# Kernel tuning notes

Measured on AMD Instinct MI355X. Metric: run time of the kernel, lower is better.

Reference implementation:

```python
import jax, jax.numpy as jnp
import numpy as np

D_MODEL = 1024
N_HEADS = 16
HEAD_DIM = D_MODEL // N_HEADS  # 64; used only as softmax scale in windowed path
WINDOW = 128


def _window_starts(seq_len, window):
    # Faithful to the torch loop: stride = window//2, last window right-aligned.
    starts = []
    for i in range(0, seq_len, window // 2):
        end = min(i + window, seq_len)
        starts.append(max(0, end - window))
        if end == seq_len:
            break
    return np.asarray(starts, dtype=np.int32)


def setup_inputs() -> dict:
    key = jax.random.key(0)
    ks = jax.random.split(key, 9)
    B, S = 4, 4096
    sc = 1.0 / np.sqrt(D_MODEL)
    return {
        "x": jax.random.normal(ks[0], (B, S, D_MODEL), jnp.float32),
        "Wq": jax.random.normal(ks[1], (D_MODEL, D_MODEL), jnp.float32) * sc,
        "bq": jax.random.normal(ks[2], (D_MODEL,), jnp.float32) * 0.02,
        "Wk": jax.random.normal(ks[3], (D_MODEL, D_MODEL), jnp.float32) * sc,
        "bk": jax.random.normal(ks[4], (D_MODEL,), jnp.float32) * 0.02,
        "Wv": jax.random.normal(ks[5], (D_MODEL, D_MODEL), jnp.float32) * sc,
        "bv": jax.random.normal(ks[6], (D_MODEL,), jnp.float32) * 0.02,
        "Wo": jax.random.normal(ks[7], (D_MODEL, D_MODEL), jnp.float32) * sc,
        "bo": jax.random.normal(ks[8], (D_MODEL,), jnp.float32) * 0.02,
    }


def reference(x, Wq, bq, Wk, bk, Wv, bv, Wo, bo):
    B, S, D = x.shape
    q = x @ Wq + bq  # [B,S,D]
    k = x @ Wk + bk
    v = x @ Wv + bv

    # Overlapping sliding windows (heads merged, as in the original windowed path).
    starts = _window_starts(S, WINDOW)                      # [W]
    idx = starts[:, None] + np.arange(WINDOW)[None, :]      # [W, w] static
    idx_j = jnp.asarray(idx)
    qw = q[:, idx_j]  # [B, W, w, D]
    kw = k[:, idx_j]
    vw = v[:, idx_j]
    scores = jnp.einsum('bwqd,bwkd->bwqk', qw, kw) / np.sqrt(HEAD_DIM)
    attn = jax.nn.softmax(scores, axis=-1)
    out_w = jnp.einsum('bwqk,bwkd->bwqd', attn, vw)         # [B, W, w, D]

    # Overlap-add then average by coverage counts.
    flat_idx = idx.reshape(-1)
    out = jnp.zeros((B, S, D), x.dtype).at[:, flat_idx].add(
        out_w.reshape(B, -1, D))
    counts = jnp.zeros((S,), x.dtype).at[flat_idx].add(1.0)
    out = out / counts[None, :, None]

    return out @ Wo + bo
```

## Files before the change

kernel.cpp:

```cpp
#include <hip/hip_runtime.h>
#include <stdint.h>
#include <stddef.h>

#define D_MODEL 1024
#define SEQ     4096
#define BATCH   4
#define MTOT    (BATCH*SEQ)
#define NWIN    63

typedef __bf16 bf16;
typedef __bf16 bf16x8 __attribute__((ext_vector_type(8)));
typedef __bf16 bf16x4 __attribute__((ext_vector_type(4)));
typedef float  floatx4 __attribute__((ext_vector_type(4)));

__device__ __forceinline__ void async_ld16(const void* g, void* l) {
  __builtin_amdgcn_global_load_lds(
      (const __attribute__((address_space(1))) unsigned int*)g,
      (__attribute__((address_space(3))) unsigned int*)l,
      16, 0, 0);
}


__global__ __launch_bounds__(256)
void cvt_x_kernel(const float* __restrict__ x, bf16* __restrict__ xb)
{
  const int i = blockIdx.x * 256 + threadIdx.x;
  const float4 v = ((const float4*)x)[i];
  bf16x4 o = { (bf16)v.x, (bf16)v.y, (bf16)v.z, (bf16)v.w };
  ((bf16x4*)xb)[i] = o;
}

__global__ __launch_bounds__(256)
void cvt_wt_kernel(const float* __restrict__ W0, const float* __restrict__ W1,
                   const float* __restrict__ W2, const float* __restrict__ W3,
                   bf16* __restrict__ wt)
{
  __shared__ float tile[32][33];
  const float* Wsel = (blockIdx.z == 0) ? W0 : (blockIdx.z == 1) ? W1
                    : (blockIdx.z == 2) ? W2 : W3;
  bf16* Wt = wt + (size_t)blockIdx.z * D_MODEL * D_MODEL;
  const int tx = threadIdx.x & 31, ty = threadIdx.x >> 5;
  const int tn = blockIdx.x * 32, tk = blockIdx.y * 32;
#pragma unroll
  for (int j = 0; j < 32; j += 8)
    tile[ty + j][tx] = Wsel[(size_t)(tk + ty + j) * D_MODEL + (tn + tx)];
  __syncthreads();
#pragma unroll
  for (int j = 0; j < 32; j += 8)
    Wt[(size_t)(tn + ty + j) * D_MODEL + (tk + tx)] = (bf16)tile[tx][ty + j];
}

__device__ __forceinline__ void gemm_core_lds(const bf16* __restrict__ A,
                                              const bf16* __restrict__ Bt,
                                              int m0, int n0,
                                              bf16* As, bf16* Bs,
                                              floatx4 (&acc)[4][4],
                                              int w, int l)
{
  const int ll = l & 15, lh = l >> 4;
  const int wm = w >> 1, wn = w & 1;

  const bf16* Abase = A  + (size_t)(m0 + ll) * D_MODEL + lh * 8;
  const bf16* Bbase = Bt + (size_t)(n0 + ll) * D_MODEL + lh * 8;

  for (int t = 0; t < 16; ++t) {
    const int k0 = t << 6;
#pragma unroll
    for (int i = 0; i < 4; ++i) {
      const int f = w * 4 + i;
      const int mt = f & 7, kk = f >> 3;
      async_ld16(Abase + (size_t)(mt * 16) * D_MODEL + (k0 + kk * 32),
                 &As[f * 512 + l * 8]);
      async_ld16(Bbase + (size_t)(mt * 16) * D_MODEL + (k0 + kk * 32),
                 &Bs[f * 512 + l * 8]);
    }
    __syncthreads();
#pragma unroll
    for (int kk = 0; kk < 2; ++kk) {
      bf16x8 af[4], bfr[4];
#pragma unroll
      for (int tt = 0; tt < 4; ++tt) {
        af[tt]  = *(const bf16x8*)&As[(kk * 8 + wm * 4 + tt) * 512 + l * 8];
        bfr[tt] = *(const bf16x8*)&Bs[(kk * 8 + wn * 4 + tt) * 512 + l * 8];
      }
#pragma unroll
      for (int mt = 0; mt < 4; ++mt)
#pragma unroll
        for (int nt = 0; nt < 4; ++nt)
          acc[mt][nt] = __builtin_amdgcn_mfma_f32_16x16x32_bf16(af[mt], bfr[nt], acc[mt][nt], 0, 0, 0);
    }
    __syncthreads();
  }
}

__global__ __launch_bounds__(256)
void gemm_qkv(const bf16* __restrict__ A, const bf16* __restrict__ Bt,
              const float* __restrict__ bq, const float* __restrict__ bk,
              const float* __restrict__ bv,
              bf16* __restrict__ qo, bf16* __restrict__ ko, bf16* __restrict__ vto)
{
  __shared__ __attribute__((aligned(16))) bf16 As[8192];
  __shared__ __attribute__((aligned(16))) bf16 Bs[8192];
  const int tid = threadIdx.x;
  const int w = tid >> 6, l = tid & 63;
  const int ll = l & 15, lh = l >> 4;
  const int wm = w >> 1, wn = w & 1;

  const int idx = blockIdx.x;
  const int xcd = idx & 7;
  const int local = idx >> 3;
  const int msub = local & 3;
  const int nblk = (local >> 2) % 24;
  const int sub  = local / 96;
  const int mblk = xcd * 16 + sub * 4 + msub;
  const int m0 = mblk * 128, n0 = nblk * 128;

  floatx4 acc[4][4];
#pragma unroll
  for (int i = 0; i < 4; ++i)
#pragma unroll
    for (int j = 0; j < 4; ++j) acc[i][j] = (floatx4)0.f;

  gemm_core_lds(A, Bt, m0, n0, As, Bs, acc, w, l);

  const int sel = n0 >> 10;
  const int ncl = n0 & 1023;
  const float* bias = (sel == 0) ? bq : (sel == 1) ? bk : bv;

#pragma unroll
  for (int mt = 0; mt < 4; ++mt) {
#pragma unroll
    for (int nt = 0; nt < 4; ++nt) {
      const int colL = ncl + wn * 64 + nt * 16 + ll;
      const float bvv = bias[colL];
#pragma unroll
      for (int r = 0; r < 4; ++r) {
        const int row = m0 + wm * 64 + mt * 16 + lh * 4 + r;
        const float v = acc[mt][nt][r] + bvv;
        if (sel == 0) {
          qo[(size_t)row * D_MODEL + colL] = (bf16)v;
        } else if (sel == 1) {
          ko[(size_t)row * D_MODEL + colL] = (bf16)v;
        } else {
          const int bb = row >> 12, s = row & 4095;
          vto[((size_t)bb * D_MODEL + colL) * SEQ + s] = (bf16)v;
        }
      }
    }
  }
}

__global__ __launch_bounds__(256)
void gemm_out(const bf16* __restrict__ A, const bf16* __restrict__ Bt,
              const float* __restrict__ bias, float* __restrict__ C)
{
  __shared__ __attribute__((aligned(16))) bf16 As[8192];
  __shared__ __attribute__((aligned(16))) bf16 Bs[8192];
  const int tid = threadIdx.x;
  const int w = tid >> 6, l = tid & 63;
  const int ll = l & 15, lh = l >> 4;
  const int wm = w >> 1, wn = w & 1;

  const int idx = blockIdx.x;
  const int xcd = idx & 7;
  const int local = idx >> 3;
  const int msub = local & 3;
  const int nblk = (local >> 2) & 7;
  const int sub  = local >> 5;
  const int mblk = xcd * 16 + sub * 4 + msub;
  const int m0 = mblk * 128, n0 = nblk * 128;

  floatx4 acc[4][4];
#pragma unroll
  for (int i = 0; i < 4; ++i)
#pragma unroll
    for (int j = 0; j < 4; ++j) acc[i][j] = (floatx4)0.f;

  gemm_core_lds(A, Bt, m0, n0, As, Bs, acc, w, l);

#pragma unroll
  for (int mt = 0; mt < 4; ++mt) {
#pragma unroll
    for (int nt = 0; nt < 4; ++nt) {
      const int col = n0 + wn * 64 + nt * 16 + ll;
      const float bvv = bias[col];
#pragma unroll
      for (int r = 0; r < 4; ++r) {
        const int row = m0 + wm * 64 + mt * 16 + lh * 4 + r;
        C[(size_t)row * D_MODEL + col] = acc[mt][nt][r] + bvv;
      }
    }
  }
}

__global__ __launch_bounds__(256)
void qk_softmax(const bf16* __restrict__ qb, const bf16* __restrict__ kb,
                bf16* __restrict__ Pg)
{
  __shared__ __attribute__((aligned(16))) bf16 As[4096];
  __shared__ __attribute__((aligned(16))) bf16 Bs[8192];
  __shared__ float redM[4][64];
  __shared__ float redS[4][64];

  const int tid = threadIdx.x;
  const int w = tid >> 6, l = tid & 63, ll = l & 15, lh = l >> 4;
  const int wh = blockIdx.x;
  const int win = wh >> 1, half = wh & 1;
  const int b = blockIdx.y;

  const bf16* Aq = qb + ((size_t)b * SEQ + win * 64 + half * 64) * D_MODEL
                 + (size_t)ll * D_MODEL + lh * 8;
  const bf16* Ak = kb + ((size_t)b * SEQ + win * 64) * D_MODEL
                 + (size_t)ll * D_MODEL + lh * 8;

  floatx4 acc[4][2];
#pragma unroll
  for (int i = 0; i < 4; ++i)
#pragma unroll
    for (int j = 0; j < 2; ++j) acc[i][j] = (floatx4)0.f;

  for (int t = 0; t < 16; ++t) {
    const int c0 = t << 6;
#pragma unroll
    for (int i = 0; i < 2; ++i) {
      const int f = w * 2 + i;
      const int mt = f & 3, kk = f >> 2;
      async_ld16(Aq + (size_t)(mt * 16) * D_MODEL + (c0 + kk * 32),
                 &As[f * 512 + l * 8]);
    }
#pragma unroll
    for (int i = 0; i < 4; ++i) {
      const int f = w * 4 + i;
      const int mt = f & 7, kk = f >> 3;
      async_ld16(Ak + (size_t)(mt * 16) * D_MODEL + (c0 + kk * 32),
                 &Bs[f * 512 + l * 8]);
    }
    __syncthreads();
#pragma unroll
    for (int kk = 0; kk < 2; ++kk) {
      bf16x8 af[4], bfr[2];
#pragma unroll
      for (int tt = 0; tt < 4; ++tt)
        af[tt]  = *(const bf16x8*)&As[(kk * 4 + tt) * 512 + l * 8];
#pragma unroll
      for (int tt = 0; tt < 2; ++tt)
        bfr[tt] = *(const bf16x8*)&Bs[(kk * 8 + w * 2 + tt) * 512 + l * 8];
#pragma unroll
      for (int mt = 0; mt < 4; ++mt)
#pragma unroll
        for (int nt = 0; nt < 2; ++nt)
          acc[mt][nt] = __builtin_amdgcn_mfma_f32_16x16x32_bf16(af[mt], bfr[nt], acc[mt][nt], 0, 0, 0);
    }
    __syncthreads();
  }

#pragma unroll
  for (int mt = 0; mt < 4; ++mt)
#pragma unroll
    for (int nt = 0; nt < 2; ++nt)
#pragma unroll
      for (int r = 0; r < 4; ++r) acc[mt][nt][r] *= 0.125f;

#pragma unroll
  for (int mt = 0; mt < 4; ++mt)
#pragma unroll
    for (int r = 0; r < 4; ++r) {
      float m = fmaxf(acc[mt][0][r], acc[mt][1][r]);
      m = fmaxf(m, __shfl_xor(m, 1));
      m = fmaxf(m, __shfl_xor(m, 2));
      m = fmaxf(m, __shfl_xor(m, 4));
      m = fmaxf(m, __shfl_xor(m, 8));
      if (ll == 0) redM[w][mt * 16 + lh * 4 + r] = m;
    }
  __syncthreads();

#pragma unroll
  for (int mt = 0; mt < 4; ++mt)
#pragma unroll
    for (int r = 0; r < 4; ++r) {
      const int row = mt * 16 + lh * 4 + r;
      const float m = fmaxf(fmaxf(redM[0][row], redM[1][row]),
                            fmaxf(redM[2][row], redM[3][row]));
      const float e0 = __expf(acc[mt][0][r] - m);
      const float e1 = __expf(acc[mt][1][r] - m);
      acc[mt][0][r] = e0; acc[mt][1][r] = e1;
      float s = e0 + e1;
      s += __shfl_xor(s, 1);
      s += __shfl_xor(s, 2);
      s += __shfl_xor(s, 4);
      s += __shfl_xor(s, 8);
      if (ll == 0) redS[w][row] = s;
    }
  __syncthreads();

  bf16* Pb = Pg + ((size_t)(b * NWIN + win) * 128 + half * 64) * 128;
#pragma unroll
  for (int mt = 0; mt < 4; ++mt)
#pragma unroll
    for (int r = 0; r < 4; ++r) {
      const int row = mt * 16 + lh * 4 + r;
      const float inv = 1.f / (redS[0][row] + redS[1][row] + redS[2][row] + redS[3][row]);
#pragma unroll
      for (int nt = 0; nt < 2; ++nt)
        Pb[(size_t)row * 128 + w * 32 + nt * 16 + ll] = (bf16)(acc[mt][nt][r] * inv);
    }
}

__global__ __launch_bounds__(256)
void pv_gather(const bf16* __restrict__ Pg, const bf16* __restrict__ vt,
               bf16* __restrict__ ab)
{
  __shared__ __attribute__((aligned(16))) bf16 As[4096];
  __shared__ __attribute__((aligned(16))) bf16 Bs[8192];

  const int tid = threadIdx.x;
  const int w = tid >> 6, l = tid & 63, ll = l & 15, lh = l >> 4;
  const int d0 = blockIdx.x * 128;
  const int h  = blockIdx.y;
  const int b  = blockIdx.z;

  int wseg[2], roff[2];
  int nseg = 0;
  if (h >= 1)        { wseg[nseg] = h - 1; roff[nseg] = 64; ++nseg; }
  if (h <= NWIN - 1) { wseg[nseg] = h;     roff[nseg] = 0;  ++nseg; }
  const float scale = (nseg == 2) ? 0.5f : 1.0f;

  floatx4 acc[4][2];
#pragma unroll
  for (int i = 0; i < 4; ++i)
#pragma unroll
    for (int j = 0; j < 2; ++j) acc[i][j] = (floatx4)0.f;

  for (int sg = 0; sg < nseg; ++sg) {
    const bf16* Pseg = Pg + ((size_t)(b * NWIN + wseg[sg]) * 128 + roff[sg]) * 128;
    const bf16* Vseg = vt + ((size_t)b * D_MODEL + d0) * SEQ + wseg[sg] * 64;
    for (int c0 = 0; c0 < 128; c0 += 64) {
#pragma unroll
      for (int i = 0; i < 2; ++i) {
        const int f = w * 2 + i;
        const int mt = f & 3, kk = f >> 2;
        async_ld16(Pseg + (size_t)(mt * 16 + ll) * 128 + (c0 + kk * 32 + lh * 8),
                   &As[f * 512 + l * 8]);
      }
#pragma unroll
      for (int i = 0; i < 4; ++i) {
        const int f = w * 4 + i;
        const int mt = f & 7, kk = f >> 3;
        async_ld16(Vseg + (size_t)(mt * 16 + ll) * SEQ + (c0 + kk * 32 + lh * 8),
                   &Bs[f * 512 + l * 8]);
      }
      __syncthreads();
#pragma unroll
      for (int kk = 0; kk < 2; ++kk) {
        bf16x8 af[4], bfr[2];
#pragma unroll
        for (int t = 0; t < 4; ++t)
          af[t]  = *(const bf16x8*)&As[(kk * 4 + t) * 512 + l * 8];
#pragma unroll
        for (int t = 0; t < 2; ++t)
          bfr[t] = *(const bf16x8*)&Bs[(kk * 8 + w * 2 + t) * 512 + l * 8];
#pragma unroll
        for (int mt = 0; mt < 4; ++mt)
#pragma unroll
          for (int nt = 0; nt < 2; ++nt)
            acc[mt][nt] = __builtin_amdgcn_mfma_f32_16x16x32_bf16(af[mt], bfr[nt], acc[mt][nt], 0, 0, 0);
      }
      __syncthreads();
    }
  }

#pragma unroll
  for (int mt = 0; mt < 4; ++mt)
#pragma unroll
    for (int nt = 0; nt < 2; ++nt)
#pragma unroll
      for (int r = 0; r < 4; ++r) {
        const int row = h * 64 + mt * 16 + lh * 4 + r;
        const int col = d0 + w * 32 + nt * 16 + ll;
        ab[((size_t)b * SEQ + row) * D_MODEL + col] = (bf16)(acc[mt][nt][r] * scale);
      }
}

extern "C" void kernel_launch(void* const* d_in, const int* in_sizes, int n_in,
                              void* d_out, int out_size, void* d_ws, size_t ws_size,
                              hipStream_t stream)
{
  (void)in_sizes; (void)n_in; (void)out_size;

  const float* x  = (const float*)d_in[0];
  const float* Wq = (const float*)d_in[1];
  const float* bq = (const float*)d_in[2];
  const float* Wk = (const float*)d_in[3];
  const float* bk = (const float*)d_in[4];
  const float* Wv = (const float*)d_in[5];
  const float* bv = (const float*)d_in[6];
  const float* Wo = (const float*)d_in[7];
  const float* bo = (const float*)d_in[8];

  if (ws_size < (size_t)176160768) return;
  char* ws = (char*)d_ws;
  bf16* xb = (bf16*)(ws);
  bf16* pb = (bf16*)(ws);
  bf16* wt = (bf16*)(ws + 33554432);
  bf16* qb = (bf16*)(ws + 41943040);
  bf16* kb = (bf16*)(ws + 75497472);
  bf16* vt = (bf16*)(ws + 109051904);
  bf16* ab = (bf16*)(ws + 142606336);

  cvt_x_kernel<<<16384, 256, 0, stream>>>(x, xb);
  cvt_wt_kernel<<<dim3(32, 32, 4), 256, 0, stream>>>(Wq, Wk, Wv, Wo, wt);

  gemm_qkv<<<3072, 256, 0, stream>>>(xb, wt, bq, bk, bv, qb, kb, vt);

  qk_softmax<<<dim3(126, BATCH), 256, 0, stream>>>(qb, kb, pb);
  pv_gather<<<dim3(8, 64, BATCH), 256, 0, stream>>>(pb, vt, ab);

  gemm_out<<<1024, 256, 0, stream>>>(ab, wt + 3145728, bo, (float*)d_out);
}
```

Measured before the change: 494.5 us.

## Double-buffer GEMM and QK loads with 256x256 tiles and 8-wave blocks

Moves the QKV and output projection GEMMs from 128x128 tiles with 4 waves to 256x256 tiles with 8 waves. K is staged in 32-wide slices through a two-buffer LDS pipeline driven by explicit vmcnt waits and barriers, and MFMA blocks are raised with setprio. The QK-softmax kernel gets the same double-buffered prefetch. This is meant to hide global-to-LDS latency and raise operand reuse. In exchange it uses more LDS and registers (32 accumulators per lane), and the grid gets much smaller: 256 blocks for the output GEMM.

```diff
diff --git a/kernel.cpp b/kernel.cpp
--- a/kernel.cpp
+++ b/kernel.cpp
@@ -50,92 +50,107 @@
     Wt[(size_t)(tn + ty + j) * D_MODEL + (tk + tx)] = (bf16)tile[tx][ty + j];
 }
 
-__device__ __forceinline__ void gemm_core_lds(const bf16* __restrict__ A,
+__device__ __forceinline__ void stage_tile(const bf16* __restrict__ Ab,
+                                           const bf16* __restrict__ Bb,
+                                           bf16* As, bf16* Bs, int t, int buf,
+                                           int w, int l)
+{
+  const int k0 = t << 5;
+  bf16* Ad = As + buf * 8192;
+  bf16* Bd = Bs + buf * 8192;
+#pragma unroll
+  for (int i = 0; i < 2; ++i) {
+    const int f = w * 2 + i;
+    async_ld16(Ab + (size_t)(f * 16) * D_MODEL + k0, Ad + f * 512 + l * 8);
+    async_ld16(Bb + (size_t)(f * 16) * D_MODEL + k0, Bd + f * 512 + l * 8);
+  }
+}
+
+__device__ __forceinline__ void gemm_core_256(const bf16* __restrict__ A,
                                               const bf16* __restrict__ Bt,
                                               int m0, int n0,
                                               bf16* As, bf16* Bs,
-                                              floatx4 (&acc)[4][4],
+                                              floatx4 (&acc)[8][4],
                                               int w, int l)
 {
   const int ll = l & 15, lh = l >> 4;
-  const int wm = w >> 1, wn = w & 1;
-
-  const bf16* Abase = A  + (size_t)(m0 + ll) * D_MODEL + lh * 8;
-  const bf16* Bbase = Bt + (size_t)(n0 + ll) * D_MODEL + lh * 8;
-
-  for (int t = 0; t < 16; ++t) {
-    const int k0 = t << 6;
-#pragma unroll
-    for (int i = 0; i < 4; ++i) {
-      const int f = w * 4 + i;
-      const int mt = f & 7, kk = f >> 3;
-      async_ld16(Abase + (size_t)(mt * 16) * D_MODEL + (k0 + kk * 32),
-                 &As[f * 512 + l * 8]);
-      async_ld16(Bbase + (size_t)(mt * 16) * D_MODEL + (k0 + kk * 32),
-                 &Bs[f * 512 + l * 8]);
-    }
-    __syncthreads();
-#pragma unroll
-    for (int kk = 0; kk < 2; ++kk) {
-      bf16x8 af[4], bfr[4];
-#pragma unroll
-      for (int tt = 0; tt < 4; ++tt) {
-        af[tt]  = *(const bf16x8*)&As[(kk * 8 + wm * 4 + tt) * 512 + l * 8];
-        bfr[tt] = *(const bf16x8*)&Bs[(kk * 8 + wn * 4 + tt) * 512 + l * 8];
-      }
-#pragma unroll
-      for (int mt = 0; mt < 4; ++mt)
-#pragma unroll
-        for (int nt = 0; nt < 4; ++nt)
-          acc[mt][nt] = __builtin_amdgcn_mfma_f32_16x16x32_bf16(af[mt], bfr[nt], acc[mt][nt], 0, 0, 0);
-    }
-    __syncthreads();
-  }
-}
-
-__global__ __launch_bounds__(256)
+  const int wm = w >> 2, wn = w & 3;
+  const bf16* Ab = A  + (size_t)(m0 + ll) * D_MODEL + lh * 8;
+  const bf16* Bb = Bt + (size_t)(n0 + ll) * D_MODEL + lh * 8;
+
+  stage_tile(Ab, Bb, As, Bs, 0, 0, w, l);
+  stage_tile(Ab, Bb, As, Bs, 1, 1, w, l);
+
+  for (int t = 0; t < 32; ++t) {
+    if (t < 31) asm volatile("s_waitcnt vmcnt(4)" ::: "memory");
+    else        asm volatile("s_waitcnt vmcnt(0)" ::: "memory");
+    __builtin_amdgcn_s_barrier();
+    __builtin_amdgcn_sched_barrier(0);
+    const bf16* Ac = As + (t & 1) * 8192;
+    const bf16* Bc = Bs + (t & 1) * 8192;
+    bf16x8 af[8], bfr[4];
+#pragma unroll
+    for (int mt = 0; mt < 8; ++mt)
+      af[mt]  = *(const bf16x8*)&Ac[(wm * 8 + mt) * 512 + l * 8];
+#pragma unroll
+    for (int nt = 0; nt < 4; ++nt)
+      bfr[nt] = *(const bf16x8*)&Bc[(wn * 4 + nt) * 512 + l * 8];
+    __builtin_amdgcn_s_setprio(1);
+#pragma unroll
+    for (int mt = 0; mt < 8; ++mt)
+#pragma unroll
+      for (int nt = 0; nt < 4; ++nt)
+        acc[mt][nt] = __builtin_amdgcn_mfma_f32_16x16x32_bf16(af[mt], bfr[nt], acc[mt][nt], 0, 0, 0);
+    __builtin_amdgcn_s_setprio(0);
+    __builtin_amdgcn_sched_barrier(0);
+    __builtin_amdgcn_s_barrier();
+    __builtin_amdgcn_sched_barrier(0);
+    if (t + 2 < 32) stage_tile(Ab, Bb, As, Bs, t + 2, t & 1, w, l);
+  }
+}
+
+__global__ __launch_bounds__(512, 2)
 void gemm_qkv(const bf16* __restrict__ A, const bf16* __restrict__ Bt,
               const float* __restrict__ bq, const float* __restrict__ bk,
               const float* __restrict__ bv,
               bf16* __restrict__ qo, bf16* __restrict__ ko, bf16* __restrict__ vto)
 {
-  __shared__ __attribute__((aligned(16))) bf16 As[8192];
-  __shared__ __attribute__((aligned(16))) bf16 Bs[8192];
+  __shared__ __attribute__((aligned(16))) bf16 As[16384];
+  __shared__ __attribute__((aligned(16))) bf16 Bs[16384];
   const int tid = threadIdx.x;
   const int w = tid >> 6, l = tid & 63;
   const int ll = l & 15, lh = l >> 4;
-  const int wm = w >> 1, wn = w & 1;
+  const int wm = w >> 2, wn = w & 3;
 
   const int idx = blockIdx.x;
   const int xcd = idx & 7;
   const int local = idx >> 3;
-  const int msub = local & 3;
-  const int nblk = (local >> 2) % 24;
-  const int sub  = local / 96;
-  const int mblk = xcd * 16 + sub * 4 + msub;
-  const int m0 = mblk * 128, n0 = nblk * 128;
-
-  floatx4 acc[4][4];
-#pragma unroll
-  for (int i = 0; i < 4; ++i)
+  const int msub = local & 7;
+  const int nblk = local >> 3;
+  const int mblk = xcd * 8 + msub;
+  const int m0 = mblk * 256, n0 = nblk * 256;
+
+  floatx4 acc[8][4];
+#pragma unroll
+  for (int i = 0; i < 8; ++i)
 #pragma unroll
     for (int j = 0; j < 4; ++j) acc[i][j] = (floatx4)0.f;
 
-  gemm_core_lds(A, Bt, m0, n0, As, Bs, acc, w, l);
+  gemm_core_256(A, Bt, m0, n0, As, Bs, acc, w, l);
 
   const int sel = n0 >> 10;
   const int ncl = n0 & 1023;
   const float* bias = (sel == 0) ? bq : (sel == 1) ? bk : bv;
 
 #pragma unroll
-  for (int mt = 0; mt < 4; ++mt) {
+  for (int mt = 0; mt < 8; ++mt) {
 #pragma unroll
     for (int nt = 0; nt < 4; ++nt) {
       const int colL = ncl + wn * 64 + nt * 16 + ll;
       const float bvv = bias[colL];
 #pragma unroll
       for (int r = 0; r < 4; ++r) {
-        const int row = m0 + wm * 64 + mt * 16 + lh * 4 + r;
+        const int row = m0 + wm * 128 + mt * 16 + lh * 4 + r;
         const float v = acc[mt][nt][r] + bvv;
         if (sel == 0) {
           qo[(size_t)row * D_MODEL + colL] = (bf16)v;
@@ -150,43 +165,42 @@
   }
 }
 
-__global__ __launch_bounds__(256)
+__global__ __launch_bounds__(512, 2)
 void gemm_out(const bf16* __restrict__ A, const bf16* __restrict__ Bt,
               const float* __restrict__ bias, float* __restrict__ C)
 {
-  __shared__ __attribute__((aligned(16))) bf16 As[8192];
-  __shared__ __attribute__((aligned(16))) bf16 Bs[8192];
+  __shared__ __attribute__((aligned(16))) bf16 As[16384];
+  __shared__ __attribute__((aligned(16))) bf16 Bs[16384];
   const int tid = threadIdx.x;
   const int w = tid >> 6, l = tid & 63;
   const int ll = l & 15, lh = l >> 4;
-  const int wm = w >> 1, wn = w & 1;
+  const int wm = w >> 2, wn = w & 3;
 
   const int idx = blockIdx.x;
   const int xcd = idx & 7;
   const int local = idx >> 3;
-  const int msub = local & 3;
-  const int nblk = (local >> 2) & 7;
-  const int sub  = local >> 5;
-  const int mblk = xcd * 16 + sub * 4 + msub;
-  const int m0 = mblk * 128, n0 = nblk * 128;
-
-  floatx4 acc[4][4];
-#pragma unroll
-  for (int i = 0; i < 4; ++i)
+  const int msub = local & 7;
+  const int nblk = local >> 3;
+  const int mblk = xcd * 8 + msub;
+  const int m0 = mblk * 256, n0 = nblk * 256;
+
+  floatx4 acc[8][4];
+#pragma unroll
+  for (int i = 0; i < 8; ++i)
 #pragma unroll
     for (int j = 0; j < 4; ++j) acc[i][j] = (floatx4)0.f;
 
-  gemm_core_lds(A, Bt, m0, n0, As, Bs, acc, w, l);
-
-#pragma unroll
-  for (int mt = 0; mt < 4; ++mt) {
+  gemm_core_256(A, Bt, m0, n0, As, Bs, acc, w, l);
+
+#pragma unroll
+  for (int mt = 0; mt < 8; ++mt) {
 #pragma unroll
     for (int nt = 0; nt < 4; ++nt) {
       const int col = n0 + wn * 64 + nt * 16 + ll;
       const float bvv = bias[col];
 #pragma unroll
       for (int r = 0; r < 4; ++r) {
-        const int row = m0 + wm * 64 + mt * 16 + lh * 4 + r;
+        const int row = m0 + wm * 128 + mt * 16 + lh * 4 + r;
         C[(size_t)row * D_MODEL + col] = acc[mt][nt][r] + bvv;
       }
     }
@@ -197,8 +211,8 @@
 void qk_softmax(const bf16* __restrict__ qb, const bf16* __restrict__ kb,
                 bf16* __restrict__ Pg)
 {
-  __shared__ __attribute__((aligned(16))) bf16 As[4096];
-  __shared__ __attribute__((aligned(16))) bf16 Bs[8192];
+  __shared__ __attribute__((aligned(16))) bf16 As[8192];
+  __shared__ __attribute__((aligned(16))) bf16 Bs[16384];
   __shared__ float redM[4][64];
   __shared__ float redS[4][64];
 
@@ -219,39 +233,57 @@
 #pragma unroll
     for (int j = 0; j < 2; ++j) acc[i][j] = (floatx4)0.f;
 
-  for (int t = 0; t < 16; ++t) {
+  auto stage = [&](int t, int buf) {
     const int c0 = t << 6;
+    bf16* Ad = As + buf * 4096;
+    bf16* Bd = Bs + buf * 8192;
 #pragma unroll
     for (int i = 0; i < 2; ++i) {
       const int f = w * 2 + i;
       const int mt = f & 3, kk = f >> 2;
       async_ld16(Aq + (size_t)(mt * 16) * D_MODEL + (c0 + kk * 32),
-                 &As[f * 512 + l * 8]);
+                 Ad + f * 512 + l * 8);
     }
 #pragma unroll
     for (int i = 0; i < 4; ++i) {
       const int f = w * 4 + i;
       const int mt = f & 7, kk = f >> 3;
       async_ld16(Ak + (size_t)(mt * 16) * D_MODEL + (c0 + kk * 32),
-                 &Bs[f * 512 + l * 8]);
-    }
-    __syncthreads();
+                 Bd + f * 512 + l * 8);
+    }
+  };
+
+  stage(0, 0);
+  stage(1, 1);
+
+  for (int t = 0; t < 16; ++t) {
+    if (t < 15) asm volatile("s_waitcnt vmcnt(6)" ::: "memory");
+    else        asm volatile("s_waitcnt vmcnt(0)" ::: "memory");
+    __builtin_amdgcn_s_barrier();
+    __builtin_amdgcn_sched_barrier(0);
+    const bf16* Ac = As + (t & 1) * 4096;
+    const bf16* Bc = Bs + (t & 1) * 8192;
 #pragma unroll
     for (int kk = 0; kk < 2; ++kk) {
       bf16x8 af[4], bfr[2];
 #pragma unroll
       for (int tt = 0; tt < 4; ++tt)
-        af[tt]  = *(const bf16x8*)&As[(kk * 4 + tt) * 512 + l * 8];
+        af[tt]  = *(const bf16x8*)&Ac[(kk * 4 + tt) * 512 + l * 8];
 #pragma unroll
       for (int tt = 0; tt < 2; ++tt)
-        bfr[tt] = *(const bf16x8*)&Bs[(kk * 8 + w * 2 + tt) * 512 + l * 8];
+        bfr[tt] = *(const bf16x8*)&Bc[(kk * 8 + w * 2 + tt) * 512 + l * 8];
+      __builtin_amdgcn_s_setprio(1);
 #pragma unroll
       for (int mt = 0; mt < 4; ++mt)
 #pragma unroll
         for (int nt = 0; nt < 2; ++nt)
           acc[mt][nt] = __builtin_amdgcn_mfma_f32_16x16x32_bf16(af[mt], bfr[nt], acc[mt][nt], 0, 0, 0);
-    }
-    __syncthreads();
+      __builtin_amdgcn_s_setprio(0);
+    }
+    __builtin_amdgcn_sched_barrier(0);
+    __builtin_amdgcn_s_barrier();
+    __builtin_amdgcn_sched_barrier(0);
+    if (t + 2 < 16) stage(t + 2, t & 1);
   }
 
 #pragma unroll
@@ -410,10 +442,10 @@
   cvt_x_kernel<<<16384, 256, 0, stream>>>(x, xb);
   cvt_wt_kernel<<<dim3(32, 32, 4), 256, 0, stream>>>(Wq, Wk, Wv, Wo, wt);
 
-  gemm_qkv<<<3072, 256, 0, stream>>>(xb, wt, bq, bk, bv, qb, kb, vt);
+  gemm_qkv<<<768, 512, 0, stream>>>(xb, wt, bq, bk, bv, qb, kb, vt);
 
   qk_softmax<<<dim3(126, BATCH), 256, 0, stream>>>(qb, kb, pb);
   pv_gather<<<dim3(8, 64, BATCH), 256, 0, stream>>>(pb, vt, ab);
 
-  gemm_out<<<1024, 256, 0, stream>>>(ab, wt + 3145728, bo, (float*)d_out);
-}
+  gemm_out<<<256, 512, 0, stream>>>(ab, wt + 3145728, bo, (float*)d_out);
+}
```

Result: faster. 441.5 us (-10.7%).

## Double-buffer LDS loads in GEMM and QK kernels with async prefetch

Applied to the files above, without the earlier changes.

Restructures the GEMM core and the QK-softmax main loop into a two-stage double-buffered pipeline. Async global-to-LDS loads for tile t+2 are issued while tile t is computed, using explicit vmcnt waits and raw barriers in place of __syncthreads. The GEMM K-step is halved to 32 so the two buffers fit in the same LDS, and the QK kernel doubles its LDS footprint. The change also raises MFMA priority with s_setprio and adds a min-blocks launch bound of 4. The goal is to hide global memory latency behind MFMA work, at the cost of more LDS and more barriers per K element in the GEMMs.

```diff
diff --git a/kernel.cpp b/kernel.cpp
--- a/kernel.cpp
+++ b/kernel.cpp
@@ -50,7 +50,7 @@
     Wt[(size_t)(tn + ty + j) * D_MODEL + (tk + tx)] = (bf16)tile[tx][ty + j];
 }
 
-__device__ __forceinline__ void gemm_core_lds(const bf16* __restrict__ A,
+__device__ __forceinline__ void gemm_core_128(const bf16* __restrict__ A,
                                               const bf16* __restrict__ Bt,
                                               int m0, int n0,
                                               bf16* As, bf16* Bs,
@@ -59,41 +59,52 @@
 {
   const int ll = l & 15, lh = l >> 4;
   const int wm = w >> 1, wn = w & 1;
-
-  const bf16* Abase = A  + (size_t)(m0 + ll) * D_MODEL + lh * 8;
-  const bf16* Bbase = Bt + (size_t)(n0 + ll) * D_MODEL + lh * 8;
-
-  for (int t = 0; t < 16; ++t) {
-    const int k0 = t << 6;
+  const bf16* Ab = A  + (size_t)(m0 + ll) * D_MODEL + lh * 8;
+  const bf16* Bb = Bt + (size_t)(n0 + ll) * D_MODEL + lh * 8;
+
+  auto stage = [&](int t, int buf) {
+    const int k0 = t << 5;
+    bf16* Ad = As + buf * 4096;
+    bf16* Bd = Bs + buf * 4096;
+#pragma unroll
+    for (int i = 0; i < 2; ++i) {
+      const int f = w * 2 + i;
+      async_ld16(Ab + (size_t)(f * 16) * D_MODEL + k0, Ad + f * 512 + l * 8);
+      async_ld16(Bb + (size_t)(f * 16) * D_MODEL + k0, Bd + f * 512 + l * 8);
+    }
+  };
+
+  stage(0, 0);
+  stage(1, 1);
+
+  for (int t = 0; t < 32; ++t) {
+    if (t < 31) asm volatile("s_waitcnt vmcnt(4)" ::: "memory");
+    else        asm volatile("s_waitcnt vmcnt(0)" ::: "memory");
+    __builtin_amdgcn_s_barrier();
+    __builtin_amdgcn_sched_barrier(0);
+    const bf16* Ac = As + (t & 1) * 4096;
+    const bf16* Bc = Bs + (t & 1) * 4096;
+    bf16x8 af[4], bfr[4];
 #pragma unroll
     for (int i = 0; i < 4; ++i) {
-      const int f = w * 4 + i;
-      const int mt = f & 7, kk = f >> 3;
-      async_ld16(Abase + (size_t)(mt * 16) * D_MODEL + (k0 + kk * 32),
-                 &As[f * 512 + l * 8]);
-      async_ld16(Bbase + (size_t)(mt * 16) * D_MODEL + (k0 + kk * 32),
-                 &Bs[f * 512 + l * 8]);
-    }
-    __syncthreads();
-#pragma unroll
-    for (int kk = 0; kk < 2; ++kk) {
-      bf16x8 af[4], bfr[4];
-#pragma unroll
-      for (int tt = 0; tt < 4; ++tt) {
-        af[tt]  = *(const bf16x8*)&As[(kk * 8 + wm * 4 + tt) * 512 + l * 8];
-        bfr[tt] = *(const bf16x8*)&Bs[(kk * 8 + wn * 4 + tt) * 512 + l * 8];
-      }
-#pragma unroll
-      for (int mt = 0; mt < 4; ++mt)
-#pragma unroll
-        for (int nt = 0; nt < 4; ++nt)
-          acc[mt][nt] = __builtin_amdgcn_mfma_f32_16x16x32_bf16(af[mt], bfr[nt], acc[mt][nt], 0, 0, 0);
-    }
-    __syncthreads();
+      af[i]  = *(const bf16x8*)&Ac[(wm * 4 + i) * 512 + l * 8];
+      bfr[i] = *(const bf16x8*)&Bc[(wn * 4 + i) * 512 + l * 8];
+    }
+    __builtin_amdgcn_s_setprio(1);
+#pragma unroll
+    for (int mt = 0; mt < 4; ++mt)
+#pragma unroll
+      for (int nt = 0; nt < 4; ++nt)
+        acc[mt][nt] = __builtin_amdgcn_mfma_f32_16x16x32_bf16(af[mt], bfr[nt], acc[mt][nt], 0, 0, 0);
+    __builtin_amdgcn_s_setprio(0);
+    __builtin_amdgcn_sched_barrier(0);
+    __builtin_amdgcn_s_barrier();
+    __builtin_amdgcn_sched_barrier(0);
+    if (t + 2 < 32) stage(t + 2, t & 1);
   }
 }
 
-__global__ __launch_bounds__(256)
+__global__ __launch_bounds__(256, 4)
 void gemm_qkv(const bf16* __restrict__ A, const bf16* __restrict__ Bt,
               const float* __restrict__ bq, const float* __restrict__ bk,
               const float* __restrict__ bv,
@@ -121,7 +132,7 @@
 #pragma unroll
     for (int j = 0; j < 4; ++j) acc[i][j] = (floatx4)0.f;
 
-  gemm_core_lds(A, Bt, m0, n0, As, Bs, acc, w, l);
+  gemm_core_128(A, Bt, m0, n0, As, Bs, acc, w, l);
 
   const int sel = n0 >> 10;
   const int ncl = n0 & 1023;
@@ -150,7 +161,7 @@
   }
 }
 
-__global__ __launch_bounds__(256)
+__global__ __launch_bounds__(256, 4)
 void gemm_out(const bf16* __restrict__ A, const bf16* __restrict__ Bt,
               const float* __restrict__ bias, float* __restrict__ C)
 {
@@ -176,7 +187,7 @@
 #pragma unroll
     for (int j = 0; j < 4; ++j) acc[i][j] = (floatx4)0.f;
 
-  gemm_core_lds(A, Bt, m0, n0, As, Bs, acc, w, l);
+  gemm_core_128(A, Bt, m0, n0, As, Bs, acc, w, l);
 
 #pragma unroll
   for (int mt = 0; mt < 4; ++mt) {
@@ -197,8 +208,8 @@
 void qk_softmax(const bf16* __restrict__ qb, const bf16* __restrict__ kb,
                 bf16* __restrict__ Pg)
 {
-  __shared__ __attribute__((aligned(16))) bf16 As[4096];
-  __shared__ __attribute__((aligned(16))) bf16 Bs[8192];
+  __shared__ __attribute__((aligned(16))) bf16 As[8192];
+  __shared__ __attribute__((aligned(16))) bf16 Bs[16384];
   __shared__ float redM[4][64];
   __shared__ float redS[4][64];
 
@@ -219,39 +230,57 @@
 #pragma unroll
     for (int j = 0; j < 2; ++j) acc[i][j] = (floatx4)0.f;
 
-  for (int t = 0; t < 16; ++t) {
+  auto stage = [&](int t, int buf) {
     const int c0 = t << 6;
+    bf16* Ad = As + buf * 4096;
+    bf16* Bd = Bs + buf * 8192;
 #pragma unroll
     for (int i = 0; i < 2; ++i) {
       const int f = w * 2 + i;
       const int mt = f & 3, kk = f >> 2;
       async_ld16(Aq + (size_t)(mt * 16) * D_MODEL + (c0 + kk * 32),
-                 &As[f * 512 + l * 8]);
+                 Ad + f * 512 + l * 8);
     }
 #pragma unroll
     for (int i = 0; i < 4; ++i) {
       const int f = w * 4 + i;
       const int mt = f & 7, kk = f >> 3;
       async_ld16(Ak + (size_t)(mt * 16) * D_MODEL + (c0 + kk * 32),
-                 &Bs[f * 512 + l * 8]);
-    }
-    __syncthreads();
+                 Bd + f * 512 + l * 8);
+    }
+  };
+
+  stage(0, 0);
+  stage(1, 1);
+
+  for (int t = 0; t < 16; ++t) {
+    if (t < 15) asm volatile("s_waitcnt vmcnt(6)" ::: "memory");
+    else        asm volatile("s_waitcnt vmcnt(0)" ::: "memory");
+    __builtin_amdgcn_s_barrier();
+    __builtin_amdgcn_sched_barrier(0);
+    const bf16* Ac = As + (t & 1) * 4096;
+    const bf16* Bc = Bs + (t & 1) * 8192;
 #pragma unroll
     for (int kk = 0; kk < 2; ++kk) {
       bf16x8 af[4], bfr[2];
 #pragma unroll
       for (int tt = 0; tt < 4; ++tt)
-        af[tt]  = *(const bf16x8*)&As[(kk * 4 + tt) * 512 + l * 8];
+        af[tt]  = *(const bf16x8*)&Ac[(kk * 4 + tt) * 512 + l * 8];
 #pragma unroll
       for (int tt = 0; tt < 2; ++tt)
-        bfr[tt] = *(const bf16x8*)&Bs[(kk * 8 + w * 2 + tt) * 512 + l * 8];
+        bfr[tt] = *(const bf16x8*)&Bc[(kk * 8 + w * 2 + tt) * 512 + l * 8];
+      __builtin_amdgcn_s_setprio(1);
 #pragma unroll
       for (int mt = 0; mt < 4; ++mt)
 #pragma unroll
         for (int nt = 0; nt < 2; ++nt)
           acc[mt][nt] = __builtin_amdgcn_mfma_f32_16x16x32_bf16(af[mt], bfr[nt], acc[mt][nt], 0, 0, 0);
-    }
-    __syncthreads();
+      __builtin_amdgcn_s_setprio(0);
+    }
+    __builtin_amdgcn_sched_barrier(0);
+    __builtin_amdgcn_s_barrier();
+    __builtin_amdgcn_sched_barrier(0);
+    if (t + 2 < 16) stage(t + 2, t & 1);
   }
 
 #pragma unroll
```

After: 482.9 us. 1.02x faster.
